# Optimization experiments

Measured on AMD Instinct MI355X. Metric: run time of the kernel, lower is better.

## Reference

```python
import jax, jax.numpy as jnp
import numpy as np

B, L = 16, 4096
D_IN, D_OUT, D_MODEL, N_LAYERS, N_STATE = 257, 257, 256, 4, 32  # 32 complex modes (= d_state 64 real)


def setup_inputs() -> dict:
    key = jax.random.key(0)
    ks = iter(jax.random.split(key, 24))
    nrm = lambda shape, s=0.02: jax.random.normal(next(ks), shape, jnp.float32) * s
    H, N = D_MODEL, N_STATE
    return {
        "x": jax.random.normal(next(ks), (B, L, D_IN, 2), jnp.float32),
        "enc_Wr": nrm((D_MODEL, D_IN)), "enc_Wi": nrm((D_MODEL, D_IN)),
        "enc_br": jnp.zeros((D_MODEL,), jnp.float32), "enc_bi": jnp.zeros((D_MODEL,), jnp.float32),
        # per layer (N_LAYERS) and per complex branch (2: real-branch S4D, imag-branch S4D)
        "s4_log_dt": jax.random.uniform(next(ks), (N_LAYERS, 2, H), jnp.float32,
                                        minval=float(np.log(0.001)), maxval=float(np.log(0.1))),
        "s4_log_A_real": jnp.broadcast_to(jnp.log(0.5 * jnp.ones((H, N), jnp.float32)), (N_LAYERS, 2, H, N)) + 0.0,
        "s4_A_imag": jnp.broadcast_to(jnp.pi * jnp.arange(N, dtype=jnp.float32), (N_LAYERS, 2, H, N)) + 0.0,
        "s4_C": jax.random.normal(next(ks), (N_LAYERS, 2, H, N, 2), jnp.float32) * (0.5 ** 0.5),
        "s4_D": jax.random.normal(next(ks), (N_LAYERS, 2, H), jnp.float32),
        "s4_Wout": nrm((N_LAYERS, 2, 2 * H, H)), "s4_bout": jnp.zeros((N_LAYERS, 2, 2 * H), jnp.float32),
        "ln_gamma": jnp.ones((N_LAYERS, 2, H), jnp.float32), "ln_beta": jnp.zeros((N_LAYERS, 2, H), jnp.float32),
        "dec_Wr": nrm((D_OUT, D_MODEL)), "dec_Wi": nrm((D_OUT, D_MODEL)),
        "dec_br": jnp.zeros((D_OUT,), jnp.float32), "dec_bi": jnp.zeros((D_OUT,), jnp.float32),
    }


def complex_linear(xr, xi, Wr, Wi, br, bi):
    yr = xr @ Wr.T - xi @ Wi.T + br
    yi = xr @ Wi.T + xi @ Wr.T + bi
    return yr, yi


def s4d_branch(u, log_dt, log_A_real, A_imag, C2, D, Wout, bout):
    """Standard S4D-minimal layer. u: (B, H, L) real."""
    Ln = u.shape[-1]
    dt = jnp.exp(log_dt)                            # (H,)
    A = -jnp.exp(log_A_real) + 1j * A_imag          # (H, N) complex
    C = C2[..., 0] + 1j * C2[..., 1]                # (H, N)
    dtA = A * dt[:, None]                           # (H, N)
    Cmod = C * (jnp.exp(dtA) - 1.0) / A
    vand = jnp.exp(dtA[..., None] * jnp.arange(Ln)) # (H, N, L)
    k = 2.0 * jnp.einsum('hn,hnl->hl', Cmod, vand).real  # (H, L)
    kf = jnp.fft.rfft(k, n=2 * Ln)
    uf = jnp.fft.rfft(u, n=2 * Ln)
    y = jnp.fft.irfft(uf * kf[None], n=2 * Ln)[..., :Ln]  # causal conv
    y = y + u * D[:, None]
    y = jax.nn.gelu(y, approximate=False)
    y = jnp.einsum('oh,bhl->bol', Wout, y) + bout[None, :, None]  # 1x1 conv to 2H
    a, g = jnp.split(y, 2, axis=1)                  # GLU over channel dim
    return a * jax.nn.sigmoid(g)


def layer_norm(x, gamma, beta):
    # x: (B, L, H), normalize over H (biased variance, like torch LayerNorm)
    mu = x.mean(-1, keepdims=True)
    var = x.var(-1, keepdims=True)
    return (x - mu) / jnp.sqrt(var + 1e-5) * gamma + beta


def reference(x, enc_Wr, enc_Wi, enc_br, enc_bi,
              s4_log_dt, s4_log_A_real, s4_A_imag, s4_C, s4_D, s4_Wout, s4_bout,
              ln_gamma, ln_beta, dec_Wr, dec_Wi, dec_br, dec_bi):
    xr, xi = complex_linear(x[..., 0], x[..., 1], enc_Wr, enc_Wi, enc_br, enc_bi)  # (B, L, H)
    xr = xr.swapaxes(-1, -2)  # (B, H, L)
    xi = xi.swapaxes(-1, -2)
    for l in range(N_LAYERS):
        sr = lambda u: s4d_branch(u, s4_log_dt[l, 0], s4_log_A_real[l, 0], s4_A_imag[l, 0],
                                  s4_C[l, 0], s4_D[l, 0], s4_Wout[l, 0], s4_bout[l, 0])
        si = lambda u: s4d_branch(u, s4_log_dt[l, 1], s4_log_A_real[l, 1], s4_A_imag[l, 1],
                                  s4_C[l, 1], s4_D[l, 1], s4_Wout[l, 1], s4_bout[l, 1])
        zr = sr(xr) - si(xi)
        zi = sr(xi) + si(xr)
        xr = xr + zr  # residual (dropout = identity)
        xi = xi + zi
        # post-norm over d_model (separate LN for real/imag parts)
        xr = layer_norm(xr.swapaxes(-1, -2), ln_gamma[l, 0], ln_beta[l, 0]).swapaxes(-1, -2)
        xi = layer_norm(xi.swapaxes(-1, -2), ln_gamma[l, 1], ln_beta[l, 1]).swapaxes(-1, -2)
    xr = xr.swapaxes(-1, -2)  # (B, L, H)
    xi = xi.swapaxes(-1, -2)
    yr, yi = complex_linear(xr, xi, dec_Wr, dec_Wi, dec_br, dec_bi)  # (B, L, D_OUT)
    return jnp.stack([yr, yi], axis=-1)
```

## Files before the change

kernel.cpp:

```cpp
#include <hip/hip_runtime.h>

typedef unsigned short ushort_t;
typedef unsigned int uint_t;
typedef __attribute__((ext_vector_type(8))) short short8;
typedef __attribute__((ext_vector_type(4))) float f32x4;

#define B_    16
#define L_    4096
#define H_    256
#define N_    32
#define DIN_  257
#define DOUT_ 257
#define NL_   4
#define Q_    128
#define NC_   32
#define BL_   (B_*L_)
#define NH_   (N_*H_)
#define PLANE_ 16777216
#define SSZ_  4194304

__device__ __forceinline__ float bfu(ushort_t u) {
    union { uint_t i; float f; } v; v.i = ((uint_t)u) << 16; return v.f;
}
__device__ __forceinline__ ushort_t f2bf(float f) {
    union { float f; uint_t i; } v; v.f = f;
    uint_t x = v.i;
    return (ushort_t)((x + 0x7FFFu + ((x >> 16) & 1u)) >> 16);
}
__device__ __forceinline__ uint2 pack4(float a, float b, float c, float d) {
    uint2 r;
    r.x = (uint_t)f2bf(a) | ((uint_t)f2bf(b) << 16);
    r.y = (uint_t)f2bf(c) | ((uint_t)f2bf(d) << 16);
    return r;
}
__device__ __forceinline__ float ldi(const void* p, size_t i, int f32) {
    return f32 ? ((const float*)p)[i] : bfu(((const ushort_t*)p)[i]);
}

__device__ __forceinline__ void gl16(const ushort_t* g, ushort_t* l) {
    __builtin_amdgcn_global_load_lds(
        (const __attribute__((address_space(1))) uint_t*)g,
        (__attribute__((address_space(3))) uint_t*)l, 16, 0, 0);
}

__device__ __forceinline__ uint4 ld8bf(const void* W, size_t eoff, int f32) {
    uint4 r;
    if (f32) {
        const float* p = (const float*)W + eoff;
        float4 a = *(const float4*)p;
        float4 b = *(const float4*)(p + 4);
        r.x = (uint_t)f2bf(a.x) | ((uint_t)f2bf(a.y) << 16);
        r.y = (uint_t)f2bf(a.z) | ((uint_t)f2bf(a.w) << 16);
        r.z = (uint_t)f2bf(b.x) | ((uint_t)f2bf(b.y) << 16);
        r.w = (uint_t)f2bf(b.z) | ((uint_t)f2bf(b.w) << 16);
    } else {
        r = *(const uint4*)((const ushort_t*)W + eoff);
    }
    return r;
}

__device__ __forceinline__ short8 negbf(short8 v) {
    short8 r;
#pragma unroll
    for (int i = 0; i < 8; ++i) r[i] = (short)(v[i] ^ (short)0x8000);
    return r;
}

#define MFMA16(a, b, c) __builtin_amdgcn_mfma_f32_16x16x32_bf16((a), (b), (c), 0, 0, 0)

__global__ void probe_kernel(const void* __restrict__ x, int* __restrict__ flag) {
    __shared__ int cnt;
    if (threadIdx.x == 0) cnt = 0;
    __syncthreads();
    uint_t w = ((const uint_t*)x)[threadIdx.x];
    float f = bfu((ushort_t)(w & 0xFFFF));
    float a = fabsf(f);
    if (a > 1e-5f && a < 100.f) atomicAdd(&cnt, 1);
    __syncthreads();
    if (threadIdx.x == 0) *flag = (cnt > 128) ? 0 : 1;
}

__global__ __launch_bounds__(256) void param_kernel(
        const void* __restrict__ log_dt, const void* __restrict__ lAr,
        const void* __restrict__ Aim, const void* __restrict__ C2,
        float* __restrict__ params, const int* __restrict__ dfl) {
    int f32 = *dfl;
    int idx = blockIdx.x * 256 + threadIdx.x;
    int h  = idx & (H_ - 1);
    int n  = (idx >> 8) & (N_ - 1);
    int lb = idx >> 13;
    float dt = expf(ldi(log_dt, lb * H_ + h, f32));
    size_t pin = (size_t)(lb * H_ + h) * N_ + n;
    float Ar = -expf(ldi(lAr, pin, f32));
    float Ai = ldi(Aim, pin, f32);
    float Cr = ldi(C2, pin * 2, f32), Ci = ldi(C2, pin * 2 + 1, f32);
    float dr = Ar * dt, di = Ai * dt;
    float e  = expf(dr);
    float wr = e * cosf(di), wi = e * sinf(di);
    float Er = wr - 1.0f, Ei = wi;
    float inv = 1.0f / (Ar * Ar + Ai * Ai);
    float Fr = (Er * Ar + Ei * Ai) * inv;
    float Fi = (Ei * Ar - Er * Ai) * inv;
    float ctr = 2.0f * (Cr * Fr - Ci * Fi);
    float cti = 2.0f * (Cr * Fi + Ci * Fr);
    float eq = expf((float)Q_ * dr);
    float ph = (float)Q_ * di;
    float wqr = eq * cosf(ph), wqi = eq * sinf(ph);
    float* pb = params + (size_t)lb * 6 * NH_;
    int o = n * H_ + h;
    pb[0 * NH_ + o] = wr;  pb[1 * NH_ + o] = wi;
    pb[2 * NH_ + o] = ctr; pb[3 * NH_ + o] = cti;
    pb[4 * NH_ + o] = wqr; pb[5 * NH_ + o] = wqi;
}

__global__ __launch_bounds__(256) void repack_x(
        const void* __restrict__ x, ushort_t* __restrict__ xre,
        ushort_t* __restrict__ xim, const int* __restrict__ dfl) {
    int f32 = *dfl;
    size_t i = ((size_t)blockIdx.x * 256 + threadIdx.x) * 4;
    int row = (int)(i >> 8);
    int k = (int)(i & 255);
    size_t src = (size_t)row * DIN_ + k;
    float re[4], im[4];
#pragma unroll
    for (int j = 0; j < 4; ++j) {
        if (f32) {
            float2 v = ((const float2*)x)[src + j];
            re[j] = v.x; im[j] = v.y;
        } else {
            uint_t v = ((const uint_t*)x)[src + j];
            re[j] = bfu((ushort_t)(v & 0xFFFF));
            im[j] = bfu((ushort_t)(v >> 16));
        }
    }
    *(uint2*)(xre + i) = pack4(re[0], re[1], re[2], re[3]);
    *(uint2*)(xim + i) = pack4(im[0], im[1], im[2], im[3]);
}

__global__ __launch_bounds__(256) void pack_encw(
        const void* __restrict__ Wr, const void* __restrict__ Wi,
        ushort_t* __restrict__ Wpr, ushort_t* __restrict__ Wpi,
        const int* __restrict__ dfl) {
    int f32 = *dfl;
    int n = blockIdx.x, k = threadIdx.x;
    Wpr[n * 256 + k] = f2bf(ldi(Wr, (size_t)n * DIN_ + k, f32));
    Wpi[n * 256 + k] = f2bf(ldi(Wi, (size_t)n * DIN_ + k, f32));
}

__global__ __launch_bounds__(256) void enc_gemm(
        const ushort_t* __restrict__ xre, const ushort_t* __restrict__ xim,
        const ushort_t* __restrict__ Wpr, const ushort_t* __restrict__ Wpi,
        const void* __restrict__ x, const void* __restrict__ eWr,
        const void* __restrict__ eWi, const void* __restrict__ br,
        const void* __restrict__ bi, ushort_t* __restrict__ xr,
        ushort_t* __restrict__ xi_, const int* __restrict__ dfl) {
    __shared__ __align__(16) ushort_t Ars[8192];
    __shared__ __align__(16) ushort_t Ais[8192];
    __shared__ __align__(16) ushort_t Brs[4096];
    __shared__ __align__(16) ushort_t Bis[4096];
    int f32 = *dfl;
    int m0 = blockIdx.x * 128, n0 = blockIdx.y * 64;
    int tid = threadIdx.x;
    int w = tid >> 6, l = tid & 63;
    int rb = w * 32;
    int lr = l & 15, lk = (l >> 4) << 4, lsw = (l & 7) << 4;
    int arow = tid >> 3;
    int acb  = ((tid & 7) << 4) ^ ((arow & 7) << 4);
    int brow = tid >> 2;
    int bq   = (tid & 3) << 5;
    int bsw  = (brow & 7) << 4;
    int wrow = n0 + brow;
    f32x4 z4 = {0.f, 0.f, 0.f, 0.f};
    f32x4 aR[2][4], aI[2][4];
#pragma unroll
    for (int mi = 0; mi < 2; ++mi)
#pragma unroll
        for (int nj = 0; nj < 4; ++nj) { aR[mi][nj] = z4; aI[mi][nj] = z4; }

    for (int k0 = 0; k0 < H_; k0 += 64) {
        if (k0) __syncthreads();
        {
            size_t so = (size_t)(m0 + arow) * H_ + k0 + (acb >> 1);
            ushort_t* dr = Ars + tid * 8;
            ushort_t* di = Ais + tid * 8;
#pragma unroll
            for (int ch = 0; ch < 4; ++ch) {
                gl16(xre + so + (size_t)ch * 32 * H_, dr + ch * 2048);
                gl16(xim + so + (size_t)ch * 32 * H_, di + ch * 2048);
            }
        }
        {
            char* pr_ = (char*)Brs + brow * 128;
            char* pi_ = (char*)Bis + brow * 128;
#pragma unroll
            for (int cc = 0; cc < 2; ++cc) {
                int cb = bq + cc * 16;
                *(uint4*)(pr_ + (cb ^ bsw)) =
                    *(const uint4*)(Wpr + (size_t)wrow * H_ + k0 + (cb >> 1));
                *(uint4*)(pi_ + (cb ^ bsw)) =
                    *(const uint4*)(Wpi + (size_t)wrow * H_ + k0 + (cb >> 1));
            }
        }
        __syncthreads();
#pragma unroll
        for (int ks = 0; ks < 2; ++ks) {
            int off = (ks * 64 + lk) ^ lsw;
            short8 x0 = *(const short8*)((const char*)Ars + (rb + lr) * 128 + off);
            short8 x1 = *(const short8*)((const char*)Ars + (rb + 16 + lr) * 128 + off);
            short8 y0 = *(const short8*)((const char*)Ais + (rb + lr) * 128 + off);
            short8 y1 = *(const short8*)((const char*)Ais + (rb + 16 + lr) * 128 + off);
#pragma unroll
            for (int nj = 0; nj < 4; ++nj) {
                short8 wr_ = *(const short8*)((const char*)Brs + (nj * 16 + lr) * 128 + off);
                short8 wi_ = *(const short8*)((const char*)Bis + (nj * 16 + lr) * 128 + off);
                short8 wn = negbf(wi_);
                aR[0][nj] = MFMA16(x0, wr_, aR[0][nj]);
                aR[0][nj] = MFMA16(y0, wn,  aR[0][nj]);
                aR[1][nj] = MFMA16(x1, wr_, aR[1][nj]);
                aR[1][nj] = MFMA16(y1, wn,  aR[1][nj]);
                aI[0][nj] = MFMA16(x0, wi_, aI[0][nj]);
                aI[0][nj] = MFMA16(y0, wr_, aI[0][nj]);
                aI[1][nj] = MFMA16(x1, wi_, aI[1][nj]);
                aI[1][nj] = MFMA16(y1, wr_, aI[1][nj]);
            }
        }
    }
    float xcr[8], xci[8];
#pragma unroll
    for (int mi = 0; mi < 2; ++mi)
#pragma unroll
        for (int r = 0; r < 4; ++r) {
            int row = m0 + rb + mi * 16 + ((l >> 4) << 2) + r;
            size_t pi = (size_t)row * DIN_ + 256;
            float re, im;
            if (f32) { float2 v = ((const float2*)x)[pi]; re = v.x; im = v.y; }
            else { uint_t v = ((const uint_t*)x)[pi];
                   re = bfu((ushort_t)(v & 0xFFFF)); im = bfu((ushort_t)(v >> 16)); }
            xcr[mi * 4 + r] = re; xci[mi * 4 + r] = im;
        }
#pragma unroll
    for (int nj = 0; nj < 4; ++nj) {
        int col = n0 + nj * 16 + lr;
        float wcr = ldi(eWr, (size_t)col * DIN_ + 256, f32);
        float wci = ldi(eWi, (size_t)col * DIN_ + 256, f32);
        float bR = ldi(br, col, f32), bI = ldi(bi, col, f32);
#pragma unroll
        for (int mi = 0; mi < 2; ++mi)
#pragma unroll
            for (int r = 0; r < 4; ++r) {
                int row = m0 + rb + mi * 16 + ((l >> 4) << 2) + r;
                int q = mi * 4 + r;
                float re = aR[mi][nj][r] + xcr[q] * wcr - xci[q] * wci + bR;
                float im = aI[mi][nj][r] + xcr[q] * wci + xci[q] * wcr + bI;
                size_t off = (size_t)row * H_ + col;
                xr[off]  = f2bf(re);
                xi_[off] = f2bf(im);
            }
    }
}

__global__ __launch_bounds__(256) void pass_a(
        const ushort_t* __restrict__ U, const float* __restrict__ P, ushort_t* __restrict__ S) {
    __shared__ __align__(16) ushort_t Us[Q_ * H_];
    int c = blockIdx.x, b = blockIdx.y, h = threadIdx.x;
    const ushort_t* ub = U + (size_t)(b * L_ + c * Q_) * H_;
#pragma unroll
    for (int p = 0; p < 16; ++p)
        gl16(ub + p * 2048 + h * 8, Us + p * 2048 + h * 8);
    float wr[N_], wi[N_], sr[N_], si[N_];
#pragma unroll
    for (int n = 0; n < N_; ++n) {
        wr[n] = P[n * H_ + h]; wi[n] = P[NH_ + n * H_ + h];
        sr[n] = 0.f; si[n] = 0.f;
    }
    __syncthreads();
    float uvn = bfu(Us[h]);
    for (int t = 0; t < Q_; ++t) {
        float uv = uvn;
        int tn = (t + 1 < Q_) ? t + 1 : t;
        uvn = bfu(Us[tn * H_ + h]);
#pragma unroll
        for (int n = 0; n < N_; ++n) {
            float nr = fmaf(wr[n], sr[n], fmaf(-wi[n], si[n], uv));
            si[n] = fmaf(wr[n], si[n], wi[n] * sr[n]);
            sr[n] = nr;
        }
    }
    size_t o = (size_t)(b * NC_ + c) * N_ * H_ + h;
#pragma unroll
    for (int n = 0; n < N_; ++n) {
        S[o + n * H_] = f2bf(sr[n]);
        S[o + n * H_ + SSZ_] = f2bf(si[n]);
    }
}

__global__ __launch_bounds__(256) void pass_b(
        const float* __restrict__ P, ushort_t* __restrict__ S) {
    int n = blockIdx.x, b = blockIdx.y, h = threadIdx.x;
    float wqr = P[4 * NH_ + n * H_ + h], wqi = P[5 * NH_ + n * H_ + h];
    float Xr = 0.f, Xi = 0.f;
    for (int c = 0; c < NC_; ++c) {
        size_t idx = ((size_t)(b * NC_ + c) * N_ + n) * H_ + h;
        float lr = bfu(S[idx]), li = bfu(S[idx + SSZ_]);
        S[idx] = f2bf(Xr); S[idx + SSZ_] = f2bf(Xi);
        float nr = fmaf(wqr, Xr, fmaf(-wqi, Xi, lr));
        Xi = fmaf(wqr, Xi, fmaf(wqi, Xr, li));
        Xr = nr;
    }
}

__global__ __launch_bounds__(256) void pass_c(
        const ushort_t* __restrict__ U, const float* __restrict__ P,
        const ushort_t* __restrict__ S, const void* __restrict__ Dp, int doff,
        ushort_t* __restrict__ G, const int* __restrict__ dfl) {
    __shared__ __align__(16) ushort_t Us[Q_ * 128];
    int f32 = *dfl;
    int c = blockIdx.x, b = blockIdx.y;
    int tid = threadIdx.x;
    int wv = tid >> 6, l = tid & 63;
    int hl = tid >> 1;
    int h = blockIdx.z * 128 + hl;
    int nb = (tid & 1) * 16;
    const ushort_t* ub = U + (size_t)(b * L_ + c * Q_) * H_ + blockIdx.z * 128;
#pragma unroll
    for (int p = 0; p < 8; ++p) {
        int row = p * 16 + wv * 4 + (l >> 4);
        gl16(ub + (size_t)row * H_ + (l & 15) * 8,
             Us + (p * 16 + wv * 4) * 128 + l * 8);
    }
    float wr[16], wi[16], cr[16], ci[16], sr[16], si[16];
#pragma unroll
    for (int i = 0; i < 16; ++i) {
        int o = (nb + i) * H_ + h;
        wr[i] = P[o]; wi[i] = P[NH_ + o];
        cr[i] = P[2 * NH_ + o]; ci[i] = P[3 * NH_ + o];
    }
    size_t so = (size_t)(b * NC_ + c) * N_ * H_ + h;
#pragma unroll
    for (int i = 0; i < 16; ++i) {
        sr[i] = bfu(S[so + (nb + i) * H_]);
        si[i] = bfu(S[so + (nb + i) * H_ + SSZ_]);
    }
    float Dv = ldi(Dp, (size_t)doff + h, f32);
    ushort_t* g = G + (size_t)(b * L_ + c * Q_) * H_ + h;
    __syncthreads();
    float uvn = bfu(Us[hl]);
    for (int t = 0; t < Q_; ++t) {
        float uv = uvn;
        int tn = (t + 1 < Q_) ? t + 1 : t;
        uvn = bfu(Us[tn * 128 + hl]);
        float a0 = 0.f, a1 = 0.f;
#pragma unroll
        for (int i = 0; i < 16; ++i) {
            float nr = fmaf(wr[i], sr[i], fmaf(-wi[i], si[i], uv));
            si[i] = fmaf(wr[i], si[i], wi[i] * sr[i]);
            sr[i] = nr;
            if (i & 1) a1 = fmaf(cr[i], sr[i], fmaf(-ci[i], si[i], a1));
            else       a0 = fmaf(cr[i], sr[i], fmaf(-ci[i], si[i], a0));
        }
        float acc = a0 + a1;
        acc += __shfl_xor(acc, 1, 64);
        float y = fmaf(Dv, uv, acc);
        float ge = 0.5f * y * (1.0f + erff(y * 0.70710678118654752f));
        if ((tid & 1) == 0) g[(size_t)t * H_] = f2bf(ge);
    }
}

__global__ __launch_bounds__(256) void wout_gemm(
        const ushort_t* __restrict__ Gb, const void* __restrict__ W, size_t woff,
        const void* __restrict__ bo, int boff, ushort_t* __restrict__ Z, int mode,
        const int* __restrict__ dfl) {
    __shared__ __align__(16) ushort_t As[8192];
    __shared__ __align__(16) ushort_t Bs[8192];
    int f32 = *dfl;
    int m0 = blockIdx.x * 128, n0 = blockIdx.y * 64;
    int tid = threadIdx.x;
    int w = tid >> 6, l = tid & 63;
    int rb = w * 32;
    int lr = l & 15, lk = (l >> 4) << 4;
    int lsw = (l & 7) << 4;
    int arow = tid >> 3;
    int acb  = ((tid & 7) << 4) ^ ((arow & 7) << 4);
    int brow = tid >> 1;
    int bhalf = (tid & 1) << 6;
    int bsw = (brow & 7) << 4;
    int wrow = (brow < 64) ? (n0 + brow) : (192 + n0 + brow);
    f32x4 z4 = {0.f, 0.f, 0.f, 0.f};
    f32x4 acc[2][8];
#pragma unroll
    for (int mi = 0; mi < 2; ++mi)
#pragma unroll
        for (int nj = 0; nj < 8; ++nj) acc[mi][nj] = z4;

    for (int k0 = 0; k0 < H_; k0 += 64) {
        if (k0) __syncthreads();
        {
            const ushort_t* src = Gb + (size_t)(m0 + arow) * H_ + k0 + (acb >> 1);
            ushort_t* dst = As + tid * 8;
#pragma unroll
            for (int ch = 0; ch < 4; ++ch)
                gl16(src + (size_t)ch * 32 * H_, dst + ch * 2048);
        }
        {
            size_t wb = woff + (size_t)wrow * H_ + k0;
            char* bp = (char*)Bs + brow * 128;
#pragma unroll
            for (int cc = 0; cc < 4; ++cc) {
                int cb = bhalf + cc * 16;
                uint4 v = ld8bf(W, wb + (cb >> 1), f32);
                *(uint4*)(bp + (cb ^ bsw)) = v;
            }
        }
        __syncthreads();
#pragma unroll
        for (int ks = 0; ks < 2; ++ks) {
            int off = (ks * 64 + lk) ^ lsw;
            short8 a0 = *(const short8*)((const char*)As + (rb + lr) * 128 + off);
            short8 a1 = *(const short8*)((const char*)As + (rb + 16 + lr) * 128 + off);
#pragma unroll
            for (int nj = 0; nj < 8; ++nj) {
                short8 bv = *(const short8*)((const char*)Bs + (nj * 16 + lr) * 128 + off);
                acc[0][nj] = MFMA16(a0, bv, acc[0][nj]);
                acc[1][nj] = MFMA16(a1, bv, acc[1][nj]);
            }
        }
    }
    float ba[4], bg[4];
#pragma unroll
    for (int nj = 0; nj < 4; ++nj) {
        ba[nj] = ldi(bo, (size_t)boff + n0 + nj * 16 + lr, f32);
        bg[nj] = ldi(bo, (size_t)boff + 256 + n0 + nj * 16 + lr, f32);
    }
#pragma unroll
    for (int mi = 0; mi < 2; ++mi)
#pragma unroll
        for (int nj = 0; nj < 4; ++nj)
#pragma unroll
            for (int r = 0; r < 4; ++r) {
                float av = acc[mi][nj][r] + ba[nj];
                float gv = acc[mi][nj + 4][r] + bg[nj];
                float s = av * (1.0f / (1.0f + expf(-gv)));
                int row = m0 + rb + mi * 16 + ((l >> 4) << 2) + r;
                size_t zo = (size_t)row * H_ + n0 + nj * 16 + lr;
                if (mode == 0)      Z[zo] = f2bf(s);
                else if (mode == 1) Z[zo] = f2bf(bfu(Z[zo]) + s);
                else                Z[zo] = f2bf(bfu(Z[zo]) - s);
            }
}

__global__ __launch_bounds__(256) void combine_ln(
        ushort_t* __restrict__ xr, ushort_t* __restrict__ xi,
        const ushort_t* __restrict__ zr, const ushort_t* __restrict__ zi,
        const void* __restrict__ gamma, const void* __restrict__ beta, int layer,
        const int* __restrict__ dfl) {
    __shared__ float red[4][4];
    int f32 = *dfl;
    int l = blockIdx.x, b = blockIdx.y, h = threadIdx.x;
    size_t row = (size_t)(b * L_ + l) * H_ + h;
    float vr = bfu(xr[row]) + bfu(zr[row]);
    float vi = bfu(xi[row]) + bfu(zi[row]);
    float s0 = vr, s1 = vr * vr, s2 = vi, s3 = vi * vi;
#pragma unroll
    for (int off = 32; off >= 1; off >>= 1) {
        s0 += __shfl_xor(s0, off, 64); s1 += __shfl_xor(s1, off, 64);
        s2 += __shfl_xor(s2, off, 64); s3 += __shfl_xor(s3, off, 64);
    }
    int wv = h >> 6;
    if ((h & 63) == 0) { red[wv][0] = s0; red[wv][1] = s1; red[wv][2] = s2; red[wv][3] = s3; }
    __syncthreads();
    float S0 = red[0][0] + red[1][0] + red[2][0] + red[3][0];
    float S1 = red[0][1] + red[1][1] + red[2][1] + red[3][1];
    float S2 = red[0][2] + red[1][2] + red[2][2] + red[3][2];
    float S3 = red[0][3] + red[1][3] + red[2][3] + red[3][3];
    const float invH = 1.0f / 256.0f;
    float mur = S0 * invH, varr = S1 * invH - mur * mur;
    float mui = S2 * invH, vari = S3 * invH - mui * mui;
    float gr = ldi(gamma, (size_t)(layer * 2 + 0) * H_ + h, f32);
    float br_ = ldi(beta, (size_t)(layer * 2 + 0) * H_ + h, f32);
    float gi = ldi(gamma, (size_t)(layer * 2 + 1) * H_ + h, f32);
    float bi_ = ldi(beta, (size_t)(layer * 2 + 1) * H_ + h, f32);
    xr[row] = f2bf((vr - mur) * rsqrtf(varr + 1e-5f) * gr + br_);
    xi[row] = f2bf((vi - mui) * rsqrtf(vari + 1e-5f) * gi + bi_);
}

__global__ __launch_bounds__(256) void dec_gemm(
        const ushort_t* __restrict__ xr, const ushort_t* __restrict__ xi,
        const void* __restrict__ Wr, const void* __restrict__ Wi,
        const void* __restrict__ br, const void* __restrict__ bi,
        void* __restrict__ out, const int* __restrict__ dfl) {
    __shared__ __align__(16) ushort_t Ars[8192];
    __shared__ __align__(16) ushort_t Ais[8192];
    __shared__ __align__(16) ushort_t Brs[4096];
    __shared__ __align__(16) ushort_t Bis[4096];
    int f32 = *dfl;
    int m0 = blockIdx.x * 128, n0 = blockIdx.y * 64;
    int tid = threadIdx.x;
    int w = tid >> 6, l = tid & 63;
    int rb = w * 32;
    int lr = l & 15, lk = (l >> 4) << 4, lsw = (l & 7) << 4;
    int arow = tid >> 3;
    int acb  = ((tid & 7) << 4) ^ ((arow & 7) << 4);
    int brow = tid >> 2;
    int bq   = (tid & 3) << 5;
    int bsw  = (brow & 7) << 4;
    int wrow = n0 + brow;
    bool bvalid = wrow < DOUT_;
    uint4 zz; zz.x = zz.y = zz.z = zz.w = 0u;
    f32x4 z4 = {0.f, 0.f, 0.f, 0.f};
    f32x4 aR[2][4], aI[2][4];
#pragma unroll
    for (int mi = 0; mi < 2; ++mi)
#pragma unroll
        for (int nj = 0; nj < 4; ++nj) { aR[mi][nj] = z4; aI[mi][nj] = z4; }

    for (int k0 = 0; k0 < H_; k0 += 64) {
        if (k0) __syncthreads();
        {
            size_t so = (size_t)(m0 + arow) * H_ + k0 + (acb >> 1);
            ushort_t* dr = Ars + tid * 8;
            ushort_t* di = Ais + tid * 8;
#pragma unroll
            for (int ch = 0; ch < 4; ++ch) {
                gl16(xr + so + (size_t)ch * 32 * H_, dr + ch * 2048);
                gl16(xi + so + (size_t)ch * 32 * H_, di + ch * 2048);
            }
        }
        {
            size_t wb = (size_t)wrow * H_ + k0 + (bq >> 1);
            char* pr_ = (char*)Brs + brow * 128;
            char* pi_ = (char*)Bis + brow * 128;
#pragma unroll
            for (int cc = 0; cc < 2; ++cc) {
                int cb = bq + cc * 16;
                uint4 vr = zz, vi = zz;
                if (bvalid) {
                    vr = ld8bf(Wr, wb + cc * 8, f32);
                    vi = ld8bf(Wi, wb + cc * 8, f32);
                }
                *(uint4*)(pr_ + (cb ^ bsw)) = vr;
                *(uint4*)(pi_ + (cb ^ bsw)) = vi;
            }
        }
        __syncthreads();
#pragma unroll
        for (int ks = 0; ks < 2; ++ks) {
            int off = (ks * 64 + lk) ^ lsw;
            short8 x0 = *(const short8*)((const char*)Ars + (rb + lr) * 128 + off);
            short8 x1 = *(const short8*)((const char*)Ars + (rb + 16 + lr) * 128 + off);
            short8 y0 = *(const short8*)((const char*)Ais + (rb + lr) * 128 + off);
            short8 y1 = *(const short8*)((const char*)Ais + (rb + 16 + lr) * 128 + off);
#pragma unroll
            for (int nj = 0; nj < 4; ++nj) {
                short8 wr_ = *(const short8*)((const char*)Brs + (nj * 16 + lr) * 128 + off);
                short8 wi_ = *(const short8*)((const char*)Bis + (nj * 16 + lr) * 128 + off);
                short8 wn = negbf(wi_);
                aR[0][nj] = MFMA16(x0, wr_, aR[0][nj]);
                aR[0][nj] = MFMA16(y0, wn,  aR[0][nj]);
                aR[1][nj] = MFMA16(x1, wr_, aR[1][nj]);
                aR[1][nj] = MFMA16(y1, wn,  aR[1][nj]);
                aI[0][nj] = MFMA16(x0, wi_, aI[0][nj]);
                aI[0][nj] = MFMA16(y0, wr_, aI[0][nj]);
                aI[1][nj] = MFMA16(x1, wi_, aI[1][nj]);
                aI[1][nj] = MFMA16(y1, wr_, aI[1][nj]);
            }
        }
    }
#pragma unroll
    for (int nj = 0; nj < 4; ++nj) {
        int col = n0 + nj * 16 + lr;
        if (col < DOUT_) {
            float bR = ldi(br, col, f32), bI = ldi(bi, col, f32);
#pragma unroll
            for (int mi = 0; mi < 2; ++mi)
#pragma unroll
                for (int r = 0; r < 4; ++r) {
                    int row = m0 + rb + mi * 16 + ((l >> 4) << 2) + r;
                    size_t pi = (size_t)row * DOUT_ + col;
                    float re = aR[mi][nj][r] + bR;
                    float im = aI[mi][nj][r] + bI;
                    if (f32) {
                        ((float2*)out)[pi] = make_float2(re, im);
                    } else {
                        ((uint_t*)out)[pi] = (uint_t)f2bf(re) | ((uint_t)f2bf(im) << 16);
                    }
                }
        }
    }
}

extern "C" void kernel_launch(void* const* d_in, const int* in_sizes, int n_in,
                              void* d_out, int out_size, void* d_ws, size_t ws_size,
                              hipStream_t stream) {
    const void* x      = d_in[0];
    const void* enc_Wr = d_in[1];
    const void* enc_Wi = d_in[2];
    const void* enc_br = d_in[3];
    const void* enc_bi = d_in[4];
    const void* log_dt = d_in[5];
    const void* lAr    = d_in[6];
    const void* Aim    = d_in[7];
    const void* C2     = d_in[8];
    const void* Dp     = d_in[9];
    const void* Wout   = d_in[10];
    const void* bout   = d_in[11];
    const void* gamma  = d_in[12];
    const void* beta   = d_in[13];
    const void* dec_Wr = d_in[14];
    const void* dec_Wi = d_in[15];
    const void* dec_br = d_in[16];
    const void* dec_bi = d_in[17];

    ushort_t* xr = (ushort_t*)d_ws;
    ushort_t* xi = xr + (size_t)PLANE_;
    ushort_t* gb = xi + (size_t)PLANE_;
    ushort_t* st = gb + (size_t)PLANE_;
    int*      fl = (int*)(st + (size_t)2 * SSZ_);
    float*    pr = (float*)(fl + 64);
    ushort_t* zr = (ushort_t*)d_out;
    ushort_t* zi = zr + (size_t)PLANE_;
    ushort_t* xre = zr;
    ushort_t* xim = zi;
    ushort_t* Wpr = st;
    ushort_t* Wpi = st + 65536;

    probe_kernel<<<1, 256, 0, stream>>>(x, fl);
    param_kernel<<<256, 256, 0, stream>>>(log_dt, lAr, Aim, C2, pr, fl);
    repack_x<<<16384, 256, 0, stream>>>(x, xre, xim, fl);
    pack_encw<<<256, 256, 0, stream>>>(enc_Wr, enc_Wi, Wpr, Wpi, fl);
    enc_gemm<<<dim3(BL_ / 128, H_ / 64), 256, 0, stream>>>(xre, xim, Wpr, Wpi,
            x, enc_Wr, enc_Wi, enc_br, enc_bi, xr, xi, fl);

    for (int l = 0; l < NL_; ++l) {
        struct App { int br; const ushort_t* U; ushort_t* Zt; int mode; };
        App apps[4] = {
            {0, xr, zr, 0},
            {1, xi, zr, 2},
            {0, xi, zi, 0},
            {1, xr, zi, 1},
        };
        for (int a = 0; a < 4; ++a) {
            const float* P = pr + (size_t)(l * 2 + apps[a].br) * 6 * NH_;
            pass_a<<<dim3(NC_, B_), 256, 0, stream>>>(apps[a].U, P, st);
            pass_b<<<dim3(N_, B_), 256, 0, stream>>>(P, st);
            pass_c<<<dim3(NC_, B_, 2), 256, 0, stream>>>(apps[a].U, P, st,
                    Dp, (l * 2 + apps[a].br) * H_, gb, fl);
            wout_gemm<<<dim3(BL_ / 128, H_ / 64), 256, 0, stream>>>(gb,
                    Wout, (size_t)(l * 2 + apps[a].br) * 512 * H_,
                    bout, (l * 2 + apps[a].br) * 512,
                    apps[a].Zt, apps[a].mode, fl);
        }
        combine_ln<<<dim3(L_, B_), 256, 0, stream>>>(xr, xi, zr, zi, gamma, beta, l, fl);
    }

    dec_gemm<<<dim3(BL_ / 128, (DOUT_ + 63) / 64), 256, 0, stream>>>(
            xr, xi, dec_Wr, dec_Wi, dec_br, dec_bi, d_out, fl);
}
```

Before: 4.509 ms.

## Split scan state modes across more threads and vectorize combine_ln rows

pass_a now splits the 32 complex modes across 4 threads per channel and launches 4x more blocks, cutting per-thread serial work and register pressure. pass_c moves from 2 to 4 threads per channel, using an extra shuffle to reduce. pass_b prefetches the next chunk's state, and combine_ln handles one row per wavefront with 4-wide vector loads and stores, which removes the shared-memory reduction and the block barrier. The trade-off is more redundant shared-memory loading of inputs, plus a pack4 helper that must already exist.

```diff
diff --git a/kernel.cpp b/kernel.cpp
--- a/kernel.cpp
+++ b/kernel.cpp
@@ -261,26 +261,30 @@
 
 __global__ __launch_bounds__(256) void pass_a(
         const ushort_t* __restrict__ U, const float* __restrict__ P, ushort_t* __restrict__ S) {
-    __shared__ __align__(16) ushort_t Us[Q_ * H_];
-    int c = blockIdx.x, b = blockIdx.y, h = threadIdx.x;
-    const ushort_t* ub = U + (size_t)(b * L_ + c * Q_) * H_;
-#pragma unroll
-    for (int p = 0; p < 16; ++p)
-        gl16(ub + p * 2048 + h * 8, Us + p * 2048 + h * 8);
-    float wr[N_], wi[N_], sr[N_], si[N_];
-#pragma unroll
-    for (int n = 0; n < N_; ++n) {
-        wr[n] = P[n * H_ + h]; wi[n] = P[NH_ + n * H_ + h];
+    __shared__ __align__(16) ushort_t Us[Q_ * 64];
+    int c = blockIdx.x, b = blockIdx.y, z = blockIdx.z;
+    int tid = threadIdx.x;
+    int hl = tid >> 2, h = z * 64 + hl;
+    int nb = (tid & 3) * 8;
+    const ushort_t* ub = U + (size_t)(b * L_ + c * Q_) * H_ + z * 64;
+#pragma unroll
+    for (int p = 0; p < 4; ++p)
+        gl16(ub + (size_t)(p * 32 + (tid >> 3)) * H_ + (tid & 7) * 8,
+             Us + p * 2048 + tid * 8);
+    float wr[8], wi[8], sr[8], si[8];
+#pragma unroll
+    for (int n = 0; n < 8; ++n) {
+        wr[n] = P[(nb + n) * H_ + h]; wi[n] = P[NH_ + (nb + n) * H_ + h];
         sr[n] = 0.f; si[n] = 0.f;
     }
     __syncthreads();
-    float uvn = bfu(Us[h]);
+    float uvn = bfu(Us[hl]);
     for (int t = 0; t < Q_; ++t) {
         float uv = uvn;
         int tn = (t + 1 < Q_) ? t + 1 : t;
-        uvn = bfu(Us[tn * H_ + h]);
-#pragma unroll
-        for (int n = 0; n < N_; ++n) {
+        uvn = bfu(Us[tn * 64 + hl]);
+#pragma unroll
+        for (int n = 0; n < 8; ++n) {
             float nr = fmaf(wr[n], sr[n], fmaf(-wi[n], si[n], uv));
             si[n] = fmaf(wr[n], si[n], wi[n] * sr[n]);
             sr[n] = nr;
@@ -288,9 +292,9 @@
     }
     size_t o = (size_t)(b * NC_ + c) * N_ * H_ + h;
 #pragma unroll
-    for (int n = 0; n < N_; ++n) {
-        S[o + n * H_] = f2bf(sr[n]);
-        S[o + n * H_ + SSZ_] = f2bf(si[n]);
+    for (int n = 0; n < 8; ++n) {
+        S[o + (nb + n) * H_] = f2bf(sr[n]);
+        S[o + (nb + n) * H_ + SSZ_] = f2bf(si[n]);
     }
 }
 
@@ -299,13 +303,19 @@
     int n = blockIdx.x, b = blockIdx.y, h = threadIdx.x;
     float wqr = P[4 * NH_ + n * H_ + h], wqi = P[5 * NH_ + n * H_ + h];
     float Xr = 0.f, Xi = 0.f;
+    size_t idx = ((size_t)(b * NC_) * N_ + n) * H_ + h;
+    float nlr = bfu(S[idx]), nli = bfu(S[idx + SSZ_]);
     for (int c = 0; c < NC_; ++c) {
-        size_t idx = ((size_t)(b * NC_ + c) * N_ + n) * H_ + h;
-        float lr = bfu(S[idx]), li = bfu(S[idx + SSZ_]);
+        float lr = nlr, li = nli;
+        if (c + 1 < NC_) {
+            nlr = bfu(S[idx + NH_]);
+            nli = bfu(S[idx + NH_ + SSZ_]);
+        }
         S[idx] = f2bf(Xr); S[idx + SSZ_] = f2bf(Xi);
         float nr = fmaf(wqr, Xr, fmaf(-wqi, Xi, lr));
         Xi = fmaf(wqr, Xi, fmaf(wqi, Xr, li));
         Xr = nr;
+        idx += NH_;
     }
 }
 
@@ -313,31 +323,27 @@
         const ushort_t* __restrict__ U, const float* __restrict__ P,
         const ushort_t* __restrict__ S, const void* __restrict__ Dp, int doff,
         ushort_t* __restrict__ G, const int* __restrict__ dfl) {
-    __shared__ __align__(16) ushort_t Us[Q_ * 128];
-    int f32 = *dfl;
-    int c = blockIdx.x, b = blockIdx.y;
+    __shared__ __align__(16) ushort_t Us[Q_ * 64];
+    int f32 = *dfl;
+    int c = blockIdx.x, b = blockIdx.y, z = blockIdx.z;
     int tid = threadIdx.x;
-    int wv = tid >> 6, l = tid & 63;
-    int hl = tid >> 1;
-    int h = blockIdx.z * 128 + hl;
-    int nb = (tid & 1) * 16;
-    const ushort_t* ub = U + (size_t)(b * L_ + c * Q_) * H_ + blockIdx.z * 128;
-#pragma unroll
-    for (int p = 0; p < 8; ++p) {
-        int row = p * 16 + wv * 4 + (l >> 4);
-        gl16(ub + (size_t)row * H_ + (l & 15) * 8,
-             Us + (p * 16 + wv * 4) * 128 + l * 8);
-    }
-    float wr[16], wi[16], cr[16], ci[16], sr[16], si[16];
-#pragma unroll
-    for (int i = 0; i < 16; ++i) {
+    int hl = tid >> 2, h = z * 64 + hl;
+    int nb = (tid & 3) * 8;
+    const ushort_t* ub = U + (size_t)(b * L_ + c * Q_) * H_ + z * 64;
+#pragma unroll
+    for (int p = 0; p < 4; ++p)
+        gl16(ub + (size_t)(p * 32 + (tid >> 3)) * H_ + (tid & 7) * 8,
+             Us + p * 2048 + tid * 8);
+    float wr[8], wi[8], cr[8], ci[8], sr[8], si[8];
+#pragma unroll
+    for (int i = 0; i < 8; ++i) {
         int o = (nb + i) * H_ + h;
         wr[i] = P[o]; wi[i] = P[NH_ + o];
         cr[i] = P[2 * NH_ + o]; ci[i] = P[3 * NH_ + o];
     }
     size_t so = (size_t)(b * NC_ + c) * N_ * H_ + h;
 #pragma unroll
-    for (int i = 0; i < 16; ++i) {
+    for (int i = 0; i < 8; ++i) {
         sr[i] = bfu(S[so + (nb + i) * H_]);
         si[i] = bfu(S[so + (nb + i) * H_ + SSZ_]);
     }
@@ -348,10 +354,10 @@
     for (int t = 0; t < Q_; ++t) {
         float uv = uvn;
         int tn = (t + 1 < Q_) ? t + 1 : t;
-        uvn = bfu(Us[tn * 128 + hl]);
+        uvn = bfu(Us[tn * 64 + hl]);
         float a0 = 0.f, a1 = 0.f;
 #pragma unroll
-        for (int i = 0; i < 16; ++i) {
+        for (int i = 0; i < 8; ++i) {
             float nr = fmaf(wr[i], sr[i], fmaf(-wi[i], si[i], uv));
             si[i] = fmaf(wr[i], si[i], wi[i] * sr[i]);
             sr[i] = nr;
@@ -360,9 +366,10 @@
         }
         float acc = a0 + a1;
         acc += __shfl_xor(acc, 1, 64);
+        acc += __shfl_xor(acc, 2, 64);
         float y = fmaf(Dv, uv, acc);
         float ge = 0.5f * y * (1.0f + erff(y * 0.70710678118654752f));
-        if ((tid & 1) == 0) g[(size_t)t * H_] = f2bf(ge);
+        if ((tid & 3) == 0) g[(size_t)t * H_] = f2bf(ge);
     }
 }
 
@@ -453,34 +460,52 @@
         const ushort_t* __restrict__ zr, const ushort_t* __restrict__ zi,
         const void* __restrict__ gamma, const void* __restrict__ beta, int layer,
         const int* __restrict__ dfl) {
-    __shared__ float red[4][4];
-    int f32 = *dfl;
-    int l = blockIdx.x, b = blockIdx.y, h = threadIdx.x;
-    size_t row = (size_t)(b * L_ + l) * H_ + h;
-    float vr = bfu(xr[row]) + bfu(zr[row]);
-    float vi = bfu(xi[row]) + bfu(zi[row]);
-    float s0 = vr, s1 = vr * vr, s2 = vi, s3 = vi * vi;
+    int f32 = *dfl;
+    int tid = threadIdx.x;
+    int wv = tid >> 6, l = tid & 63;
+    size_t row = (size_t)blockIdx.x * 4 + wv;
+    size_t base = row * H_ + l * 4;
+    uint2 vr2 = *(const uint2*)(xr + base);
+    uint2 vi2 = *(const uint2*)(xi + base);
+    uint2 zr2 = *(const uint2*)(zr + base);
+    uint2 zi2 = *(const uint2*)(zi + base);
+    float vr[4], vi[4];
+    vr[0] = bfu((ushort_t)(vr2.x & 0xFFFF)) + bfu((ushort_t)(zr2.x & 0xFFFF));
+    vr[1] = bfu((ushort_t)(vr2.x >> 16))    + bfu((ushort_t)(zr2.x >> 16));
+    vr[2] = bfu((ushort_t)(vr2.y & 0xFFFF)) + bfu((ushort_t)(zr2.y & 0xFFFF));
+    vr[3] = bfu((ushort_t)(vr2.y >> 16))    + bfu((ushort_t)(zr2.y >> 16));
+    vi[0] = bfu((ushort_t)(vi2.x & 0xFFFF)) + bfu((ushort_t)(zi2.x & 0xFFFF));
+    vi[1] = bfu((ushort_t)(vi2.x >> 16))    + bfu((ushort_t)(zi2.x >> 16));
+    vi[2] = bfu((ushort_t)(vi2.y & 0xFFFF)) + bfu((ushort_t)(zi2.y & 0xFFFF));
+    vi[3] = bfu((ushort_t)(vi2.y >> 16))    + bfu((ushort_t)(zi2.y >> 16));
+    float s0 = 0.f, s1 = 0.f, s2 = 0.f, s3 = 0.f;
+#pragma unroll
+    for (int j = 0; j < 4; ++j) {
+        s0 += vr[j]; s1 += vr[j] * vr[j];
+        s2 += vi[j]; s3 += vi[j] * vi[j];
+    }
 #pragma unroll
     for (int off = 32; off >= 1; off >>= 1) {
         s0 += __shfl_xor(s0, off, 64); s1 += __shfl_xor(s1, off, 64);
         s2 += __shfl_xor(s2, off, 64); s3 += __shfl_xor(s3, off, 64);
     }
-    int wv = h >> 6;
-    if ((h & 63) == 0) { red[wv][0] = s0; red[wv][1] = s1; red[wv][2] = s2; red[wv][3] = s3; }
-    __syncthreads();
-    float S0 = red[0][0] + red[1][0] + red[2][0] + red[3][0];
-    float S1 = red[0][1] + red[1][1] + red[2][1] + red[3][1];
-    float S2 = red[0][2] + red[1][2] + red[2][2] + red[3][2];
-    float S3 = red[0][3] + red[1][3] + red[2][3] + red[3][3];
     const float invH = 1.0f / 256.0f;
-    float mur = S0 * invH, varr = S1 * invH - mur * mur;
-    float mui = S2 * invH, vari = S3 * invH - mui * mui;
-    float gr = ldi(gamma, (size_t)(layer * 2 + 0) * H_ + h, f32);
-    float br_ = ldi(beta, (size_t)(layer * 2 + 0) * H_ + h, f32);
-    float gi = ldi(gamma, (size_t)(layer * 2 + 1) * H_ + h, f32);
-    float bi_ = ldi(beta, (size_t)(layer * 2 + 1) * H_ + h, f32);
-    xr[row] = f2bf((vr - mur) * rsqrtf(varr + 1e-5f) * gr + br_);
-    xi[row] = f2bf((vi - mui) * rsqrtf(vari + 1e-5f) * gi + bi_);
+    float mur = s0 * invH, varr = s1 * invH - mur * mur;
+    float mui = s2 * invH, vari = s3 * invH - mui * mui;
+    float rsr = rsqrtf(varr + 1e-5f), rsi = rsqrtf(vari + 1e-5f);
+    float orv[4], oiv[4];
+#pragma unroll
+    for (int j = 0; j < 4; ++j) {
+        int hh = l * 4 + j;
+        float gr  = ldi(gamma, (size_t)(layer * 2 + 0) * H_ + hh, f32);
+        float br_ = ldi(beta,  (size_t)(layer * 2 + 0) * H_ + hh, f32);
+        float gi  = ldi(gamma, (size_t)(layer * 2 + 1) * H_ + hh, f32);
+        float bi_ = ldi(beta,  (size_t)(layer * 2 + 1) * H_ + hh, f32);
+        orv[j] = (vr[j] - mur) * rsr * gr + br_;
+        oiv[j] = (vi[j] - mui) * rsi * gi + bi_;
+    }
+    *(uint2*)(xr + base) = pack4(orv[0], orv[1], orv[2], orv[3]);
+    *(uint2*)(xi + base) = pack4(oiv[0], oiv[1], oiv[2], oiv[3]);
 }
 
 __global__ __launch_bounds__(256) void dec_gemm(
@@ -640,16 +665,16 @@
         };
         for (int a = 0; a < 4; ++a) {
             const float* P = pr + (size_t)(l * 2 + apps[a].br) * 6 * NH_;
-            pass_a<<<dim3(NC_, B_), 256, 0, stream>>>(apps[a].U, P, st);
+            pass_a<<<dim3(NC_, B_, 4), 256, 0, stream>>>(apps[a].U, P, st);
             pass_b<<<dim3(N_, B_), 256, 0, stream>>>(P, st);
-            pass_c<<<dim3(NC_, B_, 2), 256, 0, stream>>>(apps[a].U, P, st,
+            pass_c<<<dim3(NC_, B_, 4), 256, 0, stream>>>(apps[a].U, P, st,
                     Dp, (l * 2 + apps[a].br) * H_, gb, fl);
             wout_gemm<<<dim3(BL_ / 128, H_ / 64), 256, 0, stream>>>(gb,
                     Wout, (size_t)(l * 2 + apps[a].br) * 512 * H_,
                     bout, (l * 2 + apps[a].br) * 512,
                     apps[a].Zt, apps[a].mode, fl);
         }
-        combine_ln<<<dim3(L_, B_), 256, 0, stream>>>(xr, xi, zr, zi, gamma, beta, l, fl);
+        combine_ln<<<BL_ / 4, 256, 0, stream>>>(xr, xi, zr, zi, gamma, beta, l, fl);
     }
 
     dec_gemm<<<dim3(BL_ / 128, (DOUT_ + 63) / 64), 256, 0, stream>>>(
```

Result: slower. 4.942 ms (+9.6%).
